# Optimization experiments

Measured on AMD Instinct MI355X. Metric: run time of the kernel, lower is better.

Reference implementation:

```python
import jax, jax.numpy as jnp
import numpy as np


def setup_inputs() -> dict:
    key = jax.random.key(0)
    ks = jax.random.split(key, 8)
    B, H, C, K, D, E, CW = 128, 100, 32, 4, 400, 200, 100
    N = B * C
    return {
        "his": jax.random.normal(ks[0], (B, H, K, D), jnp.float32),
        "cdd": jax.random.normal(ks[1], (B, C, K, D), jnp.float32),
        "channel_weight": jax.random.normal(ks[2], (N, K, CW), jnp.float32),
        "W_att": jax.random.normal(ks[3], (K, D, E), jnp.float32) * (1.0 / np.sqrt(D)),
        "b_att": jnp.zeros((K, E), jnp.float32),
        "q_att": jax.random.uniform(ks[4], (K, E), jnp.float32, -0.1, 0.1),
        "W_lin": jax.random.normal(ks[5], (D + CW, E), jnp.float32) * (1.0 / np.sqrt(D + CW)),
        "b_lin": jnp.zeros((E,), jnp.float32),
        "q_vec": jax.random.uniform(ks[6], (E,), jnp.float32, -0.1, 0.1),
    }


def reference(his, cdd, channel_weight, W_att, b_att, q_att, W_lin, b_lin, q_vec):
    B, H, K, D = his.shape
    C = cdd.shape[1]
    N = B * C

    # Per-channel additive attention over history (AdditiveAttention1 per k).
    # The original repeats his over the C candidates before attending, but the
    # attention result is independent of the candidate, so compute once per B.
    t = jnp.tanh(jnp.einsum("bhkd,kde->bkhe", his, W_att) + b_att[None, :, None, :])  # [B,K,H,E]
    a = jax.nn.softmax(jnp.einsum("bkhe,ke->bkh", t, q_att), axis=-1)                 # [B,K,H]
    u_b = jnp.einsum("bkh,bhkd->bkd", a, his)                                          # [B,K,D]

    # Broadcast to [B*C, K, D] (matches torch's repeat+view).
    u_channel = jnp.broadcast_to(u_b[:, None], (B, C, K, D)).reshape(N, K, D)

    # Per-channel candidate score: dot(u_k, cdd_k).
    cdd_flat = cdd.reshape(N, K, D)
    score = jnp.einsum("nkd,nkd->nk", u_channel, cdd_flat)[..., None]  # [N,K,1]

    # Channel-combination attention: linear + tanh + softmax over K.
    cw = jnp.concatenate([u_channel, channel_weight], axis=-1)          # [N,K,D+100]
    temp = jnp.tanh(jnp.einsum("nkf,fe->nke", cw, W_lin) + b_lin)       # [N,K,E]
    cand_w = jax.nn.softmax(jnp.einsum("nke,e->nk", temp, q_vec), axis=1)  # [N,K]

    scores = jnp.einsum("nk,nk->n", cand_w, score[..., 0])[:, None]     # [N,1]
    return scores, u_channel
```

## Files before the change

### kernel.cpp

```cpp
#include <hip/hip_runtime.h>
#include <hip/hip_bf16.h>
#include <math.h>

#define B_ 128
#define H_ 100
#define C_ 32
#define K_ 4
#define D_ 400
#define E_ 200
#define CW_ 100
#define N_ (B_*C_)
#define EPAD 224
#define DPAD 416

typedef short bf16x8 __attribute__((ext_vector_type(8)));
typedef float f32x4  __attribute__((ext_vector_type(4)));

__device__ __forceinline__ short f2b(float f) {
  union { float f; unsigned u; } x; x.f = f;
  unsigned r = x.u + 0x7fffu + ((x.u >> 16) & 1u);
  return (short)(r >> 16);
}

__global__ __launch_bounds__(256) void k0_cast(const float* __restrict__ W_att,
                                               short* __restrict__ WT) {
  const int idx = blockIdx.x * 256 + threadIdx.x;
  if (idx >= K_*EPAD*DPAD) return;
  const int d   = idx % DPAD;
  const int col = (idx / DPAD) % EPAD;
  const int k   = idx / (DPAD*EPAD);
  const float v = (d < D_ && col < E_) ? W_att[((size_t)k*D_ + d)*E_ + col] : 0.f;
  WT[idx] = f2b(v);
}

__global__ __launch_bounds__(256) void k1_mfma(const float* __restrict__ his,
                                               const short* __restrict__ WT,
                                               const float* __restrict__ b_att,
                                               const float* __restrict__ q_att,
                                               float* __restrict__ logits) {
  const int mt = blockIdx.x, k = blockIdx.y;
  const int tid = threadIdx.x;
  const int wv = tid >> 6, l = tid & 63;
  const int ln16 = l & 15, g = l >> 4;
  const int m0 = mt * 64;
  __shared__ short Al[64][40];
  __shared__ short Bl[EPAD][40];

  f32x4 acc[13];
  #pragma unroll
  for (int nt = 0; nt < 13; ++nt) acc[nt] = (f32x4){0.f, 0.f, 0.f, 0.f};

  const short* WTk = WT + (size_t)k*EPAD*DPAD;

  for (int d0 = 0; d0 < DPAD; d0 += 32) {
    __syncthreads();
    #pragma unroll
    for (int i = 0; i < 2; ++i) {
      const int idx = tid + i*256;
      const int row = idx >> 3, ch = idx & 7;
      const int d = d0 + ch*4;
      short4 s4 = {0, 0, 0, 0};
      if (d < D_) {
        const float4 a4 = *(const float4*)(his + ((size_t)(m0+row)*K_ + k)*D_ + d);
        s4.x = f2b(a4.x); s4.y = f2b(a4.y); s4.z = f2b(a4.z); s4.w = f2b(a4.w);
      }
      *(short4*)&Al[row][ch*4] = s4;
    }
    for (int idx = tid; idx < EPAD*4; idx += 256) {
      const int col = idx >> 2, ch = idx & 3;
      *(bf16x8*)&Bl[col][ch*8] = *(const bf16x8*)(WTk + (size_t)col*DPAD + d0 + ch*8);
    }
    __syncthreads();
    const bf16x8 af = *(const bf16x8*)&Al[wv*16 + ln16][g*8];
    #pragma unroll
    for (int nt = 0; nt < 13; ++nt) {
      const bf16x8 bf = *(const bf16x8*)&Bl[nt*16 + ln16][g*8];
      acc[nt] = __builtin_amdgcn_mfma_f32_16x16x32_bf16(af, bf, acc[nt], 0, 0, 0);
    }
  }

  float p[4] = {0.f, 0.f, 0.f, 0.f};
  #pragma unroll
  for (int nt = 0; nt < 13; ++nt) {
    const int e = nt*16 + ln16;
    float q = 0.f, bb = 0.f;
    if (e < E_) { q = q_att[k*E_ + e]; bb = b_att[k*E_ + e]; }
    #pragma unroll
    for (int reg = 0; reg < 4; ++reg)
      p[reg] += tanhf(acc[nt][reg] + bb) * q;
  }
  #pragma unroll
  for (int off = 1; off < 16; off <<= 1)
    #pragma unroll
    for (int reg = 0; reg < 4; ++reg) p[reg] += __shfl_xor(p[reg], off);
  if (ln16 == 0) {
    #pragma unroll
    for (int reg = 0; reg < 4; ++reg) {
      const int m = m0 + wv*16 + g*4 + reg;
      const int b = m / H_, h = m % H_;
      logits[(b*K_ + k)*H_ + h] = p[reg];
    }
  }
}

__global__ __launch_bounds__(512) void k2_fused(const float* __restrict__ his,
                                                const float* __restrict__ logits,
                                                const float* __restrict__ W_lin,
                                                const float* __restrict__ b_lin,
                                                float* __restrict__ u_b,
                                                float* __restrict__ ulin) {
  const int b = blockIdx.x, k = blockIdx.y;
  const int tid = threadIdx.x;
  __shared__ float sv[128];
  __shared__ float sa[H_];
  __shared__ float4 part[4][100];
  __shared__ float ul[D_];

  float v = -INFINITY;
  if (tid < H_) v = logits[(b*K_ + k)*H_ + tid];
  if (tid < 128) sv[tid] = v;
  __syncthreads();
  for (int s = 64; s > 0; s >>= 1) { if (tid < s) sv[tid] = fmaxf(sv[tid], sv[tid+s]); __syncthreads(); }
  const float mx = sv[0];
  __syncthreads();
  const float ev = (tid < H_) ? expf(v - mx) : 0.f;
  if (tid < 128) sv[tid] = ev;
  __syncthreads();
  for (int s = 64; s > 0; s >>= 1) { if (tid < s) sv[tid] += sv[tid+s]; __syncthreads(); }
  const float inv = 1.f / sv[0];
  if (tid < H_) sa[tid] = ev * inv;
  __syncthreads();

  const int gg = tid / 100;
  const int d4 = tid % 100;
  if (tid < 400) {
    float4 a4 = {0.f, 0.f, 0.f, 0.f};
    const float* hp = his + (((size_t)b*H_ + gg*25)*K_ + k)*D_ + d4*4;
    #pragma unroll 5
    for (int h = 0; h < 25; ++h) {
      const float4 x = *(const float4*)(hp + (size_t)h*K_*D_);
      const float w = sa[gg*25 + h];
      a4.x += w*x.x; a4.y += w*x.y; a4.z += w*x.z; a4.w += w*x.w;
    }
    part[gg][d4] = a4;
  }
  __syncthreads();
  if (tid < 100) {
    const float4 p0 = part[0][tid], p1 = part[1][tid], p2 = part[2][tid], p3 = part[3][tid];
    float4 a4;
    a4.x = p0.x+p1.x+p2.x+p3.x; a4.y = p0.y+p1.y+p2.y+p3.y;
    a4.z = p0.z+p1.z+p2.z+p3.z; a4.w = p0.w+p1.w+p2.w+p3.w;
    *(float4*)&ul[tid*4] = a4;
    *(float4*)(u_b + ((size_t)b*K_ + k)*D_ + tid*4) = a4;
  }
  __syncthreads();

  if (tid < E_) {
    float a0 = b_lin[tid], a1 = 0.f, a2 = 0.f, a3 = 0.f;
    #pragma unroll 2
    for (int d = 0; d < D_; d += 4) {
      a0 += ul[d]   * W_lin[(size_t)d*E_     + tid];
      a1 += ul[d+1] * W_lin[(size_t)(d+1)*E_ + tid];
      a2 += ul[d+2] * W_lin[(size_t)(d+2)*E_ + tid];
      a3 += ul[d+3] * W_lin[(size_t)(d+3)*E_ + tid];
    }
    ulin[((size_t)b*K_ + k)*E_ + tid] = a0 + a1 + a2 + a3;
  }
}

__global__ __launch_bounds__(256) void k4_score(const float* __restrict__ cdd,
                                                const float* __restrict__ cwt,
                                                const float* __restrict__ W_lin,
                                                const float* __restrict__ q_vec,
                                                const float* __restrict__ u_b,
                                                const float* __restrict__ ulin,
                                                float* __restrict__ out) {
  const int n = blockIdx.x;
  const int b = n >> 5;
  const int tid = threadIdx.x;
  const int wv = tid >> 6, ln = tid & 63;
  __shared__ float cw[K_][CW_];
  __shared__ float red[4][K_];
  __shared__ float sc[K_];

  for (int idx = tid; idx < K_*CW_; idx += 256)
    cw[idx / CW_][idx % CW_] = cwt[(size_t)n*K_*CW_ + idx];
  __syncthreads();

  {
    const float4* up = (const float4*)(u_b + ((size_t)b*K_ + wv)*D_);
    const float4* cp = (const float4*)(cdd + ((size_t)n*K_ + wv)*D_);
    float s = 0.f;
    for (int dd = ln; dd < 100; dd += 64) {
      const float4 u = up[dd], c = cp[dd];
      s += u.x*c.x + u.y*c.y + u.z*c.z + u.w*c.w;
    }
    #pragma unroll
    for (int off = 32; off >= 1; off >>= 1) s += __shfl_down(s, off);
    if (ln == 0) sc[wv] = s;
  }

  float pl0 = 0.f, pl1 = 0.f, pl2 = 0.f, pl3 = 0.f;
  if (tid < E_) {
    const int e = tid;
    float a0 = 0.f, a1 = 0.f, a2 = 0.f, a3 = 0.f;
    #pragma unroll 4
    for (int c = 0; c < CW_; ++c) {
      const float w = W_lin[(size_t)(D_ + c)*E_ + e];
      a0 += cw[0][c]*w; a1 += cw[1][c]*w; a2 += cw[2][c]*w; a3 += cw[3][c]*w;
    }
    const float q = q_vec[e];
    const float* ue = ulin + (size_t)b*K_*E_ + e;
    pl0 = tanhf(ue[0*E_] + a0) * q;
    pl1 = tanhf(ue[1*E_] + a1) * q;
    pl2 = tanhf(ue[2*E_] + a2) * q;
    pl3 = tanhf(ue[3*E_] + a3) * q;
  }
  #pragma unroll
  for (int off = 1; off < 64; off <<= 1) {
    pl0 += __shfl_xor(pl0, off); pl1 += __shfl_xor(pl1, off);
    pl2 += __shfl_xor(pl2, off); pl3 += __shfl_xor(pl3, off);
  }
  if (ln == 0) { red[wv][0] = pl0; red[wv][1] = pl1; red[wv][2] = pl2; red[wv][3] = pl3; }
  __syncthreads();

  if (tid == 0) {
    const float l0 = red[0][0]+red[1][0]+red[2][0]+red[3][0];
    const float l1 = red[0][1]+red[1][1]+red[2][1]+red[3][1];
    const float l2 = red[0][2]+red[1][2]+red[2][2]+red[3][2];
    const float l3 = red[0][3]+red[1][3]+red[2][3]+red[3][3];
    const float m = fmaxf(fmaxf(l0, l1), fmaxf(l2, l3));
    const float e0 = expf(l0 - m), e1 = expf(l1 - m);
    const float e2 = expf(l2 - m), e3 = expf(l3 - m);
    const float s = e0 + e1 + e2 + e3;
    out[n] = (e0*sc[0] + e1*sc[1] + e2*sc[2] + e3*sc[3]) / s;
  }

  {
    const float4* ub4 = (const float4*)(u_b + (size_t)b*K_*D_);
    float4* uo = (float4*)(out + N_ + (size_t)n*K_*D_);
    for (int idx = tid; idx < 400; idx += 256) uo[idx] = ub4[idx];
  }
}

extern "C" void kernel_launch(void* const* d_in, const int* in_sizes, int n_in,
                              void* d_out, int out_size, void* d_ws, size_t ws_size,
                              hipStream_t stream) {
  const float* his   = (const float*)d_in[0];
  const float* cdd   = (const float*)d_in[1];
  const float* cwt   = (const float*)d_in[2];
  const float* W_att = (const float*)d_in[3];
  const float* b_att = (const float*)d_in[4];
  const float* q_att = (const float*)d_in[5];
  const float* W_lin = (const float*)d_in[6];
  const float* b_lin = (const float*)d_in[7];
  const float* q_vec = (const float*)d_in[8];
  float* out = (float*)d_out;

  float* ws     = (float*)d_ws;
  float* logits = ws;
  float* u_b    = ws + (size_t)B_*K_*H_;
  float* ulin   = u_b + (size_t)B_*K_*D_;
  short* WT     = (short*)(ulin + (size_t)B_*K_*E_);

  k0_cast  <<<(K_*EPAD*DPAD + 255)/256, 256, 0, stream>>>(W_att, WT);
  k1_mfma  <<<dim3((B_*H_)/64, K_), 256, 0, stream>>>(his, WT, b_att, q_att, logits);
  k2_fused <<<dim3(B_, K_),         512, 0, stream>>>(his, logits, W_lin, b_lin, u_b, ulin);
  k4_score <<<N_,                   256, 0, stream>>>(cdd, cwt, W_lin, q_vec, u_b, ulin, out);
}
```

Measured before the change: 282.7 us.

## Fuse attention-logit MFMA GEMM into per-(b,k) softmax/pooling kernel with double buffering

Merges the bf16 MFMA logit GEMM into the softmax/weighted-sum kernel, so each (b,k) block computes its own 100-row logits directly into shared memory and skips the logits round trip through global memory and one launch. The weight cast kernel now writes W_att pre-tiled into padded 208x40 chunks, which lets the fused kernel stream the chunks straight to LDS with global_load_lds while the next his chunk is prefetched in double buffers. The cost is a grid of only 512 blocks with 112 padded rows, so 7 of the 8 waves do the MFMA work and the rest idle, plus heavier LDS use per block that may reduce occupancy.

```diff
diff --git a/kernel.cpp b/kernel.cpp
--- a/kernel.cpp
+++ b/kernel.cpp
@@ -10,8 +10,9 @@
 #define E_ 200
 #define CW_ 100
 #define N_ (B_*C_)
-#define EPAD 224
-#define DPAD 416
+#define NCH 13
+#define NTI 13
+#define MR_ 112
 
 typedef short bf16x8 __attribute__((ext_vector_type(8)));
 typedef float f32x4  __attribute__((ext_vector_type(4)));
@@ -22,102 +23,136 @@
   return (short)(r >> 16);
 }
 
+__device__ __forceinline__ void gload_lds16(const void* g, void* l) {
+  __builtin_amdgcn_global_load_lds((const __attribute__((address_space(1))) void*)g,
+                                   (__attribute__((address_space(3))) void*)l, 16, 0, 0);
+}
+
 __global__ __launch_bounds__(256) void k0_cast(const float* __restrict__ W_att,
                                                short* __restrict__ WT) {
-  const int idx = blockIdx.x * 256 + threadIdx.x;
-  if (idx >= K_*EPAD*DPAD) return;
-  const int d   = idx % DPAD;
-  const int col = (idx / DPAD) % EPAD;
-  const int k   = idx / (DPAD*EPAD);
-  const float v = (d < D_ && col < E_) ? W_att[((size_t)k*D_ + d)*E_ + col] : 0.f;
-  WT[idx] = f2b(v);
-}
-
-__global__ __launch_bounds__(256) void k1_mfma(const float* __restrict__ his,
-                                               const short* __restrict__ WT,
-                                               const float* __restrict__ b_att,
-                                               const float* __restrict__ q_att,
-                                               float* __restrict__ logits) {
-  const int mt = blockIdx.x, k = blockIdx.y;
+  const int k = blockIdx.x, c = blockIdx.y;
   const int tid = threadIdx.x;
-  const int wv = tid >> 6, l = tid & 63;
-  const int ln16 = l & 15, g = l >> 4;
-  const int m0 = mt * 64;
-  __shared__ short Al[64][40];
-  __shared__ short Bl[EPAD][40];
-
-  f32x4 acc[13];
-  #pragma unroll
-  for (int nt = 0; nt < 13; ++nt) acc[nt] = (f32x4){0.f, 0.f, 0.f, 0.f};
-
-  const short* WTk = WT + (size_t)k*EPAD*DPAD;
-
-  for (int d0 = 0; d0 < DPAD; d0 += 32) {
-    __syncthreads();
-    #pragma unroll
-    for (int i = 0; i < 2; ++i) {
-      const int idx = tid + i*256;
-      const int row = idx >> 3, ch = idx & 7;
-      const int d = d0 + ch*4;
-      short4 s4 = {0, 0, 0, 0};
-      if (d < D_) {
-        const float4 a4 = *(const float4*)(his + ((size_t)(m0+row)*K_ + k)*D_ + d);
-        s4.x = f2b(a4.x); s4.y = f2b(a4.y); s4.z = f2b(a4.z); s4.w = f2b(a4.w);
-      }
-      *(short4*)&Al[row][ch*4] = s4;
-    }
-    for (int idx = tid; idx < EPAD*4; idx += 256) {
-      const int col = idx >> 2, ch = idx & 3;
-      *(bf16x8*)&Bl[col][ch*8] = *(const bf16x8*)(WTk + (size_t)col*DPAD + d0 + ch*8);
-    }
-    __syncthreads();
-    const bf16x8 af = *(const bf16x8*)&Al[wv*16 + ln16][g*8];
-    #pragma unroll
-    for (int nt = 0; nt < 13; ++nt) {
-      const bf16x8 bf = *(const bf16x8*)&Bl[nt*16 + ln16][g*8];
-      acc[nt] = __builtin_amdgcn_mfma_f32_16x16x32_bf16(af, bf, acc[nt], 0, 0, 0);
-    }
-  }
-
-  float p[4] = {0.f, 0.f, 0.f, 0.f};
-  #pragma unroll
-  for (int nt = 0; nt < 13; ++nt) {
-    const int e = nt*16 + ln16;
-    float q = 0.f, bb = 0.f;
-    if (e < E_) { q = q_att[k*E_ + e]; bb = b_att[k*E_ + e]; }
-    #pragma unroll
-    for (int reg = 0; reg < 4; ++reg)
-      p[reg] += tanhf(acc[nt][reg] + bb) * q;
-  }
-  #pragma unroll
-  for (int off = 1; off < 16; off <<= 1)
-    #pragma unroll
-    for (int reg = 0; reg < 4; ++reg) p[reg] += __shfl_xor(p[reg], off);
-  if (ln16 == 0) {
-    #pragma unroll
-    for (int reg = 0; reg < 4; ++reg) {
-      const int m = m0 + wv*16 + g*4 + reg;
-      const int b = m / H_, h = m % H_;
-      logits[(b*K_ + k)*H_ + h] = p[reg];
-    }
-  }
-}
-
-__global__ __launch_bounds__(512) void k2_fused(const float* __restrict__ his,
-                                                const float* __restrict__ logits,
-                                                const float* __restrict__ W_lin,
-                                                const float* __restrict__ b_lin,
-                                                float* __restrict__ u_b,
-                                                float* __restrict__ ulin) {
+  __shared__ float Wst[32][200];
+  for (int idx = tid; idx < 32*200; idx += 256) {
+    const int j = idx / 200, col = idx % 200;
+    const int d = c*32 + j;
+    Wst[j][col] = (d < D_) ? W_att[((size_t)k*D_ + d)*E_ + col] : 0.f;
+  }
+  __syncthreads();
+  short* dst = WT + (size_t)(k*NCH + c)*208*40;
+  for (int idx = tid; idx < 208*40; idx += 256) {
+    const int col = idx / 40, j = idx % 40;
+    const float v = (col < E_ && j < 32) ? Wst[j][col] : 0.f;
+    dst[idx] = f2b(v);
+  }
+}
+
+__global__ __launch_bounds__(512) void k12_fused(const float* __restrict__ his,
+                                                 const short* __restrict__ WT,
+                                                 const float* __restrict__ b_att,
+                                                 const float* __restrict__ q_att,
+                                                 const float* __restrict__ W_lin,
+                                                 const float* __restrict__ b_lin,
+                                                 float* __restrict__ u_b,
+                                                 float* __restrict__ ulin) {
   const int b = blockIdx.x, k = blockIdx.y;
   const int tid = threadIdx.x;
+  const int w = tid >> 6, l = tid & 63;
+  const int ln16 = l & 15, g = l >> 4;
+
+  __shared__ __align__(16) short Al[2][MR_][40];
+  __shared__ __align__(16) short Bl[2][208][40];
+  __shared__ float sl[MR_];
   __shared__ float sv[128];
   __shared__ float sa[H_];
   __shared__ float4 part[4][100];
   __shared__ float ul[D_];
 
-  float v = -INFINITY;
-  if (tid < H_) v = logits[(b*K_ + k)*H_ + tid];
+  f32x4 acc[NTI];
+  #pragma unroll
+  for (int nt = 0; nt < NTI; ++nt) acc[nt] = (f32x4){0.f, 0.f, 0.f, 0.f};
+
+  const int arow = tid >> 2, aq = tid & 3;
+  const bool astage = (tid < 448);
+  const float* hisrow = his + (((size_t)b*H_ + arow)*K_ + k)*D_;
+  const short* WTk = WT + (size_t)k*NCH*208*40;
+
+  float4 a0, a1;
+  {
+    const int d = 0 + aq*8;
+    a0 = (float4){0,0,0,0}; a1 = a0;
+    if (astage && arow < H_ && d < D_) {
+      a0 = *(const float4*)(hisrow + d);
+      a1 = *(const float4*)(hisrow + d + 4);
+    }
+    const short* src = WTk;
+    for (int i = tid; i < 1040; i += 512)
+      gload_lds16(src + i*8, (short*)&Bl[0][0][0] + i*8);
+    if (astage) {
+      short s8[8];
+      s8[0]=f2b(a0.x); s8[1]=f2b(a0.y); s8[2]=f2b(a0.z); s8[3]=f2b(a0.w);
+      s8[4]=f2b(a1.x); s8[5]=f2b(a1.y); s8[6]=f2b(a1.z); s8[7]=f2b(a1.w);
+      *(bf16x8*)&Al[0][arow][aq*8] = *(bf16x8*)s8;
+    }
+  }
+  __syncthreads();
+
+  int buf = 0;
+  for (int c = 0; c < NCH; ++c) {
+    const int nb = buf ^ 1;
+    const bool more = (c + 1 < NCH);
+    if (more) {
+      const int d = (c+1)*32 + aq*8;
+      a0 = (float4){0,0,0,0}; a1 = a0;
+      if (astage && arow < H_ && d < D_) {
+        a0 = *(const float4*)(hisrow + d);
+        a1 = *(const float4*)(hisrow + d + 4);
+      }
+      const short* src = WTk + (size_t)(c+1)*208*40;
+      for (int i = tid; i < 1040; i += 512)
+        gload_lds16(src + i*8, (short*)&Bl[nb][0][0] + i*8);
+    }
+    if (w < 7) {
+      const bf16x8 af = *(const bf16x8*)&Al[buf][w*16 + ln16][g*8];
+      #pragma unroll
+      for (int nt = 0; nt < NTI; ++nt) {
+        const bf16x8 bf = *(const bf16x8*)&Bl[buf][nt*16 + ln16][g*8];
+        acc[nt] = __builtin_amdgcn_mfma_f32_16x16x32_bf16(af, bf, acc[nt], 0, 0, 0);
+      }
+    }
+    if (more && astage) {
+      short s8[8];
+      s8[0]=f2b(a0.x); s8[1]=f2b(a0.y); s8[2]=f2b(a0.z); s8[3]=f2b(a0.w);
+      s8[4]=f2b(a1.x); s8[5]=f2b(a1.y); s8[6]=f2b(a1.z); s8[7]=f2b(a1.w);
+      *(bf16x8*)&Al[nb][arow][aq*8] = *(bf16x8*)s8;
+    }
+    __syncthreads();
+    buf = nb;
+  }
+
+  if (w < 7) {
+    float p[4] = {0.f, 0.f, 0.f, 0.f};
+    #pragma unroll
+    for (int nt = 0; nt < NTI; ++nt) {
+      const int e = nt*16 + ln16;
+      float q = 0.f, bb = 0.f;
+      if (e < E_) { q = q_att[k*E_ + e]; bb = b_att[k*E_ + e]; }
+      #pragma unroll
+      for (int reg = 0; reg < 4; ++reg)
+        p[reg] += tanhf(acc[nt][reg] + bb) * q;
+    }
+    #pragma unroll
+    for (int off = 1; off < 16; off <<= 1)
+      #pragma unroll
+      for (int reg = 0; reg < 4; ++reg) p[reg] += __shfl_xor(p[reg], off);
+    if (ln16 == 0) {
+      #pragma unroll
+      for (int reg = 0; reg < 4; ++reg) sl[w*16 + g*4 + reg] = p[reg];
+    }
+  }
+  __syncthreads();
+
+  const float v = (tid < H_) ? sl[tid] : -INFINITY;
   if (tid < 128) sv[tid] = v;
   __syncthreads();
   for (int s = 64; s > 0; s >>= 1) { if (tid < s) sv[tid] = fmaxf(sv[tid], sv[tid+s]); __syncthreads(); }
@@ -131,16 +166,15 @@
   if (tid < H_) sa[tid] = ev * inv;
   __syncthreads();
 
-  const int gg = tid / 100;
-  const int d4 = tid % 100;
+  const int gg = tid / 100, d4 = tid % 100;
   if (tid < 400) {
     float4 a4 = {0.f, 0.f, 0.f, 0.f};
     const float* hp = his + (((size_t)b*H_ + gg*25)*K_ + k)*D_ + d4*4;
     #pragma unroll 5
     for (int h = 0; h < 25; ++h) {
       const float4 x = *(const float4*)(hp + (size_t)h*K_*D_);
-      const float w = sa[gg*25 + h];
-      a4.x += w*x.x; a4.y += w*x.y; a4.z += w*x.z; a4.w += w*x.w;
+      const float ww = sa[gg*25 + h];
+      a4.x += ww*x.x; a4.y += ww*x.y; a4.z += ww*x.z; a4.w += ww*x.w;
     }
     part[gg][d4] = a4;
   }
@@ -156,15 +190,15 @@
   __syncthreads();
 
   if (tid < E_) {
-    float a0 = b_lin[tid], a1 = 0.f, a2 = 0.f, a3 = 0.f;
+    float c0 = b_lin[tid], c1 = 0.f, c2 = 0.f, c3 = 0.f;
     #pragma unroll 2
     for (int d = 0; d < D_; d += 4) {
-      a0 += ul[d]   * W_lin[(size_t)d*E_     + tid];
-      a1 += ul[d+1] * W_lin[(size_t)(d+1)*E_ + tid];
-      a2 += ul[d+2] * W_lin[(size_t)(d+2)*E_ + tid];
-      a3 += ul[d+3] * W_lin[(size_t)(d+3)*E_ + tid];
-    }
-    ulin[((size_t)b*K_ + k)*E_ + tid] = a0 + a1 + a2 + a3;
+      c0 += ul[d]   * W_lin[(size_t)d*E_     + tid];
+      c1 += ul[d+1] * W_lin[(size_t)(d+1)*E_ + tid];
+      c2 += ul[d+2] * W_lin[(size_t)(d+2)*E_ + tid];
+      c3 += ul[d+3] * W_lin[(size_t)(d+3)*E_ + tid];
+    }
+    ulin[((size_t)b*K_ + k)*E_ + tid] = c0 + c1 + c2 + c3;
   }
 }
 
@@ -257,14 +291,12 @@
   const float* q_vec = (const float*)d_in[8];
   float* out = (float*)d_out;
 
-  float* ws     = (float*)d_ws;
-  float* logits = ws;
-  float* u_b    = ws + (size_t)B_*K_*H_;
-  float* ulin   = u_b + (size_t)B_*K_*D_;
-  short* WT     = (short*)(ulin + (size_t)B_*K_*E_);
-
-  k0_cast  <<<(K_*EPAD*DPAD + 255)/256, 256, 0, stream>>>(W_att, WT);
-  k1_mfma  <<<dim3((B_*H_)/64, K_), 256, 0, stream>>>(his, WT, b_att, q_att, logits);
-  k2_fused <<<dim3(B_, K_),         512, 0, stream>>>(his, logits, W_lin, b_lin, u_b, ulin);
-  k4_score <<<N_,                   256, 0, stream>>>(cdd, cwt, W_lin, q_vec, u_b, ulin, out);
-}
+  float* ws   = (float*)d_ws;
+  float* u_b  = ws;
+  float* ulin = u_b + (size_t)B_*K_*D_;
+  short* WT   = (short*)(ulin + (size_t)B_*K_*E_);
+
+  k0_cast  <<<dim3(K_, NCH),  256, 0, stream>>>(W_att, WT);
+  k12_fused<<<dim3(B_, K_),   512, 0, stream>>>(his, WT, b_att, q_att, W_lin, b_lin, u_b, ulin);
+  k4_score <<<N_,             256, 0, stream>>>(cdd, cwt, W_lin, q_vec, u_b, ulin, out);
+}
```

After: 252.2 us. 10.8% less time.
